# Optimization experiments

Hardware: AMD Instinct MI355X
Metric: run time of the kernel (lower is better)

The kernel has to match this reference:

```python
import jax, jax.numpy as jnp
import numpy as np

B, C, WS, HK = 32, 384, 7, 8           # batch, channels, window size, windows per side
NB, NH, HID = 2, 12, 1536              # num blocks, heads, mlp hidden (4*C)
H = W = HK * WS                        # 56
EPS = 1e-6


def _rel_pos_index(ws: int) -> np.ndarray:
    # Replicates the torch loop: tmp[dy-y+off, dx-x+off] with python negative-index wrap.
    rd = 2 * ws - 1
    a = np.arange(ws)
    qy, qx, ky, kx = np.meshgrid(a, a, a, a, indexing='ij')
    idx = ((ky - qy + ws // 2) % rd) * rd + ((kx - qx + ws // 2) % rd)
    return idx.reshape(ws * ws, ws * ws)


def setup_inputs() -> dict:
    key = jax.random.key(0)
    ks = jax.random.split(key, 12)
    s = 0.02
    inp = {
        'cls_tokens': jax.random.normal(ks[0], (B, C, HK, HK), jnp.float32),
        'patch_tokens': jax.random.normal(ks[1], (B, C, H, W), jnp.float32),
        'qkv_w': s * jax.random.normal(ks[2], (NB, 3 * C, C), jnp.float32),
        'qkv_b': jnp.zeros((NB, 3 * C), jnp.float32),
        'proj_w': s * jax.random.normal(ks[3], (NB, C, C), jnp.float32),
        'proj_b': jnp.zeros((NB, C), jnp.float32),
        'rel_pos': s * jax.random.normal(ks[4], (NB, NH, (2 * WS - 1) ** 2), jnp.float32),
        'ln0_w': jnp.ones((NB, C), jnp.float32), 'ln0_b': jnp.zeros((NB, C), jnp.float32),
        'ln1_w': jnp.ones((NB, C), jnp.float32), 'ln1_b': jnp.zeros((NB, C), jnp.float32),
        'ln2_w': jnp.ones((NB, C), jnp.float32), 'ln2_b': jnp.zeros((NB, C), jnp.float32),
        'mlp_w1': s * jax.random.normal(ks[5], (NB, HID, C), jnp.float32),
        'mlp_b1': jnp.zeros((NB, HID), jnp.float32),
        'mlp_w2': s * jax.random.normal(ks[6], (NB, C, HID), jnp.float32),
        'mlp_b2': jnp.zeros((NB, C), jnp.float32),
    }
    return inp


def _ln(x, w, b):
    m = x.mean(-1, keepdims=True)
    v = ((x - m) ** 2).mean(-1, keepdims=True)
    return (x - m) * jax.lax.rsqrt(v + EPS) * w + b


def _forward(cls_tokens, patch_tokens, qkv_w, qkv_b, proj_w, proj_b, rel_pos,
             ln0_w, ln0_b, ln1_w, ln1_b, ln2_w, ln2_b, mlp_w1, mlp_b1, mlp_w2, mlp_b2):
    hd = C // NH
    scale = hd ** -0.5
    NP = WS * WS  # patch tokens per window

    idx = _rel_pos_index(WS)                                 # [49,49] static
    rp = rel_pos[:, :, idx.reshape(-1)].reshape(NB, NH, NP, NP)
    rp = jnp.pad(rp, ((0, 0), (0, 0), (1, 0), (1, 0)))       # zero bias on cls row/col

    # Projection is Identity (in==out channels, pool=False).
    # convert_to_flatten_layout (no padding needed: H % (HK*WS) == 0)
    p = patch_tokens.reshape(B, C, HK, WS, HK, WS).transpose(0, 2, 4, 3, 5, 1)
    p = p.reshape(B * HK * HK, NP, C)                        # [Bw, 49, C]
    c = cls_tokens.transpose(0, 2, 3, 1).reshape(B * HK * HK, 1, C)
    out = jnp.concatenate([c, p], axis=1)                    # [Bw, 50, C]

    def attn(x, i, patch_attn):
        bx, n, _ = x.shape
        qkv = (x @ qkv_w[i].T + qkv_b[i]).reshape(bx, n, 3, NH, hd).transpose(2, 0, 3, 1, 4)
        q, k, v = qkv[0], qkv[1], qkv[2]
        a = jnp.einsum('bhnd,bhmd->bhnm', q, k) * scale
        if patch_attn:
            a = a + rp[i]
        a = jax.nn.softmax(a, axis=-1)
        o = jnp.einsum('bhnm,bhmd->bhnd', a, v).transpose(0, 2, 1, 3).reshape(bx, n, C)
        return o @ proj_w[i].T + proj_b[i]

    for i in range(NB):
        # cls-token (region) attention across windows of one image
        ct = out[:, 0:1, :].reshape(B, HK * HK, C)
        ct = ct + attn(_ln(ct, ln0_w[i], ln0_b[i]), i, False)
        out = jnp.concatenate([ct.reshape(-1, 1, C), out[:, 1:, :]], axis=1)
        # windowed attention with rel-pos bias
        out = out + attn(_ln(out, ln1_w[i], ln1_b[i]), i, True)
        # MLP (expand is Identity since in==out channels)
        h = _ln(out, ln2_w[i], ln2_b[i])
        h = jax.nn.gelu(h @ mlp_w1[i].T + mlp_b1[i], approximate=False)
        out = out + (h @ mlp_w2[i].T + mlp_b2[i])

    # convert_to_spatial_layout
    cls_out = out[:, 0].reshape(B, HK, HK, C).transpose(0, 3, 1, 2)
    patch_out = out[:, 1:].reshape(B, HK, HK, WS, WS, C).transpose(0, 5, 1, 3, 2, 4).reshape(B, C, H, W)
    return cls_out, patch_out


def reference(cls_tokens, patch_tokens, qkv_w, qkv_b, proj_w, proj_b, rel_pos,
              ln0_w, ln0_b, ln1_w, ln1_b, ln2_w, ln2_b, mlp_w1, mlp_b1, mlp_w2, mlp_b2):
    return _forward(cls_tokens, patch_tokens, qkv_w, qkv_b, proj_w, proj_b, rel_pos,
                    ln0_w, ln0_b, ln1_w, ln1_b, ln2_w, ln2_b, mlp_w1, mlp_b1, mlp_w2, mlp_b2)
```

## Files before the change

kernel.cpp:

```cpp
#include <hip/hip_runtime.h>
#include <hip/hip_bf16.h>
#include <cstdint>
#include <cstddef>

#define BB    32
#define CC    384
#define NHH   12
#define HDD   32
#define WSS   7
#define HKK   8
#define NBB   2
#define HIDD  1536
#define NTT   50
#define NWW   2048
#define LDOUT 19200
#define N3    1152

typedef __attribute__((ext_vector_type(8))) short short8v;
typedef __attribute__((ext_vector_type(4))) float f32x4;

#if defined(__has_builtin)
#if __has_builtin(__builtin_amdgcn_global_load_lds)
#define HAS_GLDS 1
#endif
#endif
#ifndef HAS_GLDS
#define HAS_GLDS 0
#endif

static __device__ __forceinline__ float gelu_f(float x) {
    float t = x * (0.7978845608028654f + 0.03567740814f * x * x);
    float e = __expf(2.0f * t);
    float th = 1.0f - 2.0f / (e + 1.0f);
    return 0.5f * x * (1.0f + th);
}

static __device__ __forceinline__ short bf16s(float x) {
    __hip_bfloat16 b = __float2bfloat16(x);
    return *(short*)&b;
}

static __device__ __forceinline__ float bf2f(short s) {
    union { unsigned int u; float f; } cv;
    cv.u = ((unsigned int)(unsigned short)s) << 16;
    return cv.f;
}

#if HAS_GLDS
static __device__ __forceinline__ void glds16(const short* g, short* l) {
    __builtin_amdgcn_global_load_lds(
        (const __attribute__((address_space(1))) unsigned int*)g,
        (__attribute__((address_space(3))) unsigned int*)l,
        16, 0, 0);
}
#endif

static __device__ __forceinline__ void swz_decode(int L, int nx, int ny, int& bx, int& by) {
    if (ny & 7) {
        bx = L % nx; by = L / nx;
    } else {
        int r = L & 7, pos = L >> 3;
        bx = pos % nx;
        by = (pos / nx) * 8 + r;
    }
}

__global__ void pack_cls_kernel(const float* __restrict__ cls, __hip_bfloat16* __restrict__ out) {
    __shared__ float lds[64][65];
    int bid = blockIdx.x;
    int b = bid / 6, cc = bid % 6, c0 = cc * 64;
    int tid = threadIdx.x;
    for (int idx = tid; idx < 64 * 64; idx += 256) {
        int k = idx & 63, cl = idx >> 6;
        lds[cl][k] = cls[((size_t)b * CC + c0 + cl) * 64 + k];
    }
    __syncthreads();
    short* ob = (short*)out;
    for (int idx = tid; idx < 64 * 64; idx += 256) {
        int cl = idx & 63, k = idx >> 6;
        ob[(size_t)(b * 64 + k) * LDOUT + c0 + cl] = bf16s(lds[cl][k]);
    }
}

__global__ void pack_patch_kernel(const float* __restrict__ patch, __hip_bfloat16* __restrict__ out) {
    __shared__ float lds[64][57];
    int bid = blockIdx.x;
    int b = bid / 336, rem = bid % 336;
    int y = rem / 6, cc = rem % 6, c0 = cc * 64;
    int tid = threadIdx.x;
    for (int idx = tid; idx < 64 * 56; idx += 256) {
        int cl = idx / 56, x = idx % 56;
        lds[cl][x] = patch[(((size_t)b * CC + c0 + cl) * 56 + y) * 56 + x];
    }
    __syncthreads();
    int wsy = y % 7, hky = y / 7;
    short* ob = (short*)out;
    for (int idx = tid; idx < 64 * 56; idx += 256) {
        int cl = idx & 63, x = idx >> 6;
        int tok = 1 + wsy * 7 + (x % 7);
        int win = b * 64 + hky * 8 + (x / 7);
        ob[((size_t)win * NTT + tok) * CC + c0 + cl] = bf16s(lds[cl][x]);
    }
}

__global__ void unpack_cls_kernel(const __hip_bfloat16* __restrict__ out, float* __restrict__ cls_out) {
    __shared__ float lds[64][65];
    int bid = blockIdx.x;
    int b = bid / 6, cc = bid % 6, c0 = cc * 64;
    int tid = threadIdx.x;
    const short* ob = (const short*)out;
    for (int idx = tid; idx < 64 * 64; idx += 256) {
        int cl = idx & 63, k = idx >> 6;
        lds[cl][k] = bf2f(ob[(size_t)(b * 64 + k) * LDOUT + c0 + cl]);
    }
    __syncthreads();
    for (int idx = tid; idx < 64 * 64; idx += 256) {
        int k = idx & 63, cl = idx >> 6;
        cls_out[((size_t)b * CC + c0 + cl) * 64 + k] = lds[cl][k];
    }
}

__global__ void unpack_patch_kernel(const __hip_bfloat16* __restrict__ out, float* __restrict__ patch_out) {
    __shared__ float lds[64][57];
    int bid = blockIdx.x;
    int b = bid / 336, rem = bid % 336;
    int y = rem / 6, cc = rem % 6, c0 = cc * 64;
    int tid = threadIdx.x;
    int wsy = y % 7, hky = y / 7;
    const short* ob = (const short*)out;
    for (int idx = tid; idx < 64 * 56; idx += 256) {
        int cl = idx & 63, x = idx >> 6;
        int tok = 1 + wsy * 7 + (x % 7);
        int win = b * 64 + hky * 8 + (x / 7);
        lds[cl][x] = bf2f(ob[((size_t)win * NTT + tok) * CC + c0 + cl]);
    }
    __syncthreads();
    for (int idx = tid; idx < 64 * 56; idx += 256) {
        int cl = idx / 56, x = idx % 56;
        patch_out[((size_t)b * CC + c0 + cl) * 3136 + y * 56 + x] = lds[cl][x];
    }
}

__global__ void f2bf_kernel(const float* __restrict__ in, __hip_bfloat16* __restrict__ out, int n) {
    int i = (blockIdx.x * 256 + threadIdx.x) * 4;
    if (i + 3 < n) {
        float4 v = *(const float4*)(in + i);
        out[i + 0] = __float2bfloat16(v.x);
        out[i + 1] = __float2bfloat16(v.y);
        out[i + 2] = __float2bfloat16(v.z);
        out[i + 3] = __float2bfloat16(v.w);
    } else {
        for (; i < n; ++i) out[i] = __float2bfloat16(in[i]);
    }
}

__global__ void bias_precompute_kernel(const float* __restrict__ rp, float* __restrict__ biasT) {
    int h = blockIdx.x;
    for (int idx = threadIdx.x; idx < 4096; idx += 256) {
        int qt = idx >> 6, kt = idx & 63;
        float v = 0.f;
        if (qt >= 1 && qt < NTT && kt >= 1 && kt < NTT) {
            int qp = qt - 1, kp = kt - 1;
            int qy = qp / 7, qx = qp - qy * 7;
            int ky = kp / 7, kx = kp - ky * 7;
            int ridx = ((ky - qy + 16) % 13) * 13 + ((kx - qx + 16) % 13);
            v = rp[h * 169 + ridx];
        }
        biasT[h * 4096 + qt * 64 + (kt & 15) * 4 + (kt >> 4)] = v;
    }
}

__global__ void ln_kernel(const __hip_bfloat16* __restrict__ x, int ldx,
                          const float* __restrict__ w, const float* __restrict__ b,
                          __hip_bfloat16* __restrict__ y, int ldy, int M) {
    int wave = threadIdx.x >> 6, lane = threadIdx.x & 63;
    int row = blockIdx.x * 4 + wave;
    if (row >= M) return;
    const ushort2* xr = (const ushort2*)((const short*)x + (size_t)row * ldx);
    float2 vals[3];
    float s = 0.f;
#pragma unroll
    for (int j = 0; j < 3; ++j) {
        ushort2 u = xr[lane + j * 64];
        vals[j].x = bf2f((short)u.x);
        vals[j].y = bf2f((short)u.y);
        s += vals[j].x + vals[j].y;
    }
#pragma unroll
    for (int off = 32; off > 0; off >>= 1) s += __shfl_xor(s, off);
    float mean = s * (1.0f / 384.0f);
    float vs = 0.f;
#pragma unroll
    for (int j = 0; j < 3; ++j) {
        float dx = vals[j].x - mean, dy = vals[j].y - mean;
        vs += dx * dx + dy * dy;
    }
#pragma unroll
    for (int off = 32; off > 0; off >>= 1) vs += __shfl_xor(vs, off);
    float inv = rsqrtf(vs * (1.0f / 384.0f) + 1e-6f);
    const float2* w2 = (const float2*)w;
    const float2* b2 = (const float2*)b;
    ushort* yr = (ushort*)y + (size_t)row * ldy;
#pragma unroll
    for (int j = 0; j < 3; ++j) {
        int c = lane + j * 64;
        float2 wv = w2[c], bv = b2[c];
        ushort2 o;
        o.x = (ushort)bf16s((vals[j].x - mean) * inv * wv.x + bv.x);
        o.y = (ushort)bf16s((vals[j].y - mean) * inv * wv.y + bv.y);
        *(ushort2*)(yr + c * 2) = o;
    }
}

template <int BIAS, int GELU, int ACC>
__global__ __launch_bounds__(512, 4) void gemm_bf16_kernel(
    const __hip_bfloat16* __restrict__ A, int lda,
    const __hip_bfloat16* __restrict__ W,
    const float* __restrict__ bias,
    __hip_bfloat16* __restrict__ Yb, int ldyb,
    int M, int N, int K, int nx) {
    __shared__ __align__(16) union SMemU {
        struct { short As[3][256 * 32]; short Bs[3][128 * 32]; } st;
        short obf[256][132];
    } sm;
    int tid = threadIdx.x;
    int lane = tid & 63;
    int wid = tid >> 6;
    int wr = wid >> 1, wc = wid & 1;
    int bx, by;
    swz_decode(blockIdx.x, nx, M >> 8, bx, by);
    int row0 = by * 256, col0 = bx * 128;

    const short* Ag = (const short*)A + (size_t)(row0 + wid * 32 + (lane >> 2)) * lda + (lane & 3) * 8;
    const short* Wg = (const short*)W + (size_t)(col0 + wid * 16 + (lane >> 2)) * K + (lane & 3) * 8;
    size_t astep16 = (size_t)16 * lda;
    int ldsA = wid * 32 * 32;
    int ldsB = wid * 16 * 32;

#if HAS_GLDS
#define STAGE(buf, k0)                                                \
    do {                                                              \
        glds16(Ag + (k0), &sm.st.As[buf][ldsA]);                      \
        glds16(Ag + astep16 + (k0), &sm.st.As[buf][ldsA + 16 * 32]);  \
        glds16(Wg + (k0), &sm.st.Bs[buf][ldsB]);                      \
    } while (0)
#else
#define STAGE(buf, k0)                                                               \
    do {                                                                             \
        *(short8v*)(&sm.st.As[buf][ldsA] + lane * 8) = *(const short8v*)(Ag + (k0)); \
        *(short8v*)(&sm.st.As[buf][ldsA + 16 * 32] + lane * 8) = *(const short8v*)(Ag + astep16 + (k0)); \
        *(short8v*)(&sm.st.Bs[buf][ldsB] + lane * 8) = *(const short8v*)(Wg + (k0)); \
    } while (0)
#endif

    f32x4 acc[4][4] = {};
    int frow_a = wr * 64 + (lane & 15);
    int frow_b = wc * 64 + (lane & 15);
    int fk = (lane >> 4) * 8;

    int nt = K >> 5;
#if HAS_GLDS
    STAGE(0, 0);
    if (nt > 1) STAGE(1, 32);
    int sc = 0;
    for (int t = 0; t < nt; ++t) {
        int sn = sc + 2; if (sn >= 3) sn -= 3;
        if (t + 2 < nt) {
            STAGE(sn, (t + 2) << 5);
            asm volatile("s_waitcnt vmcnt(6)" ::: "memory");
        } else if (t + 1 < nt) {
            asm volatile("s_waitcnt vmcnt(3)" ::: "memory");
        } else {
            asm volatile("s_waitcnt vmcnt(0)" ::: "memory");
        }
        __builtin_amdgcn_s_barrier();
        __builtin_amdgcn_sched_barrier(0);
        short8v a[4], b[4];
#pragma unroll
        for (int m = 0; m < 4; ++m) a[m] = *(const short8v*)&sm.st.As[sc][(frow_a + m * 16) * 32 + fk];
#pragma unroll
        for (int n = 0; n < 4; ++n) b[n] = *(const short8v*)&sm.st.Bs[sc][(frow_b + n * 16) * 32 + fk];
        __builtin_amdgcn_s_setprio(1);
#pragma unroll
        for (int m = 0; m < 4; ++m)
#pragma unroll
            for (int n = 0; n < 4; ++n)
                acc[m][n] = __builtin_amdgcn_mfma_f32_16x16x32_bf16(a[m], b[n], acc[m][n], 0, 0, 0);
        __builtin_amdgcn_s_setprio(0);
        __builtin_amdgcn_sched_barrier(0);
        __builtin_amdgcn_s_barrier();
        ++sc; if (sc >= 3) sc = 0;
    }
#else
    STAGE(0, 0);
    __syncthreads();
    int cur = 0;
    for (int t = 0; t < nt; ++t) {
        if (t + 1 < nt) STAGE(cur ^ 1, (t + 1) << 5);
        short8v a[4], b[4];
#pragma unroll
        for (int m = 0; m < 4; ++m) a[m] = *(const short8v*)&sm.st.As[cur][(frow_a + m * 16) * 32 + fk];
#pragma unroll
        for (int n = 0; n < 4; ++n) b[n] = *(const short8v*)&sm.st.Bs[cur][(frow_b + n * 16) * 32 + fk];
#pragma unroll
        for (int m = 0; m < 4; ++m)
#pragma unroll
            for (int n = 0; n < 4; ++n)
                acc[m][n] = __builtin_amdgcn_mfma_f32_16x16x32_bf16(a[m], b[n], acc[m][n], 0, 0, 0);
        if (t + 1 < nt) { __syncthreads(); cur ^= 1; }
    }
#endif
#undef STAGE

    __syncthreads();
    int lr = (lane >> 4) * 4;
    int lc = lane & 15;
#pragma unroll
    for (int n = 0; n < 4; ++n) {
        int c = wc * 64 + n * 16 + lc;
        float bv = BIAS ? bias[col0 + c] : 0.0f;
#pragma unroll
        for (int m = 0; m < 4; ++m) {
#pragma unroll
            for (int j = 0; j < 4; ++j) {
                float v = acc[m][n][j] + bv;
                if (GELU) v = gelu_f(v);
                sm.obf[wr * 64 + m * 16 + lr + j][c] = bf16s(v);
            }
        }
    }
    __syncthreads();
    short* yb = (short*)Yb + (size_t)row0 * ldyb + col0;
#pragma unroll
    for (int it = 0; it < 8; ++it) {
        int r = (tid >> 4) + it * 32;
        int c8 = (tid & 15) * 8;
        short8v v = *(const short8v*)&sm.obf[r][c8];
        short* yp = yb + (size_t)r * ldyb + c8;
        if (ACC) {
            short8v o = *(const short8v*)yp;
#pragma unroll
            for (int e = 0; e < 8; ++e) v[e] = bf16s(bf2f(v[e]) + bf2f(o[e]));
        }
        *(short8v*)yp = v;
    }
}

__global__ __launch_bounds__(256) void attn_mfma_kernel(
    const __hip_bfloat16* __restrict__ qkv,
    const float* __restrict__ biasT,
    __hip_bfloat16* __restrict__ o,
    int T, float scale, int nwin) {
    __shared__ __align__(16) short Vt[4][32][72];
    __shared__ __align__(16) short Pl[4][64][40];
    const int tid = threadIdx.x, lane = tid & 63, wv = tid >> 6;
    int p, hg;
    {
        int L = blockIdx.x;
        if (nwin & 7) { hg = L % 3; p = L / 3; }
        else { int r = L & 7, pos = L >> 3; hg = pos % 3; p = (pos / 3) * 8 + r; }
    }
    const int h = hg * 4 + wv;
    const short* q_base = (const short*)qkv + (size_t)p * T * N3;

    const int fr = lane & 15;
    const int fk = (lane >> 4) * 8;
    const int lg = lane >> 4;
    const int lc = lane & 15;

    short8v aq[4], bk[4];
#pragma unroll
    for (int m = 0; m < 4; ++m) {
        const short* qp = q_base + (size_t)(m * 16 + fr) * N3 + h * 32 + fk;
        aq[m] = *(const short8v*)qp;
        bk[m] = *(const short8v*)(qp + 384);
    }

    for (int ch = lane; ch < T * 4; ch += 64) {
        int t = ch >> 2, cq = ch & 3;
        short8v v8 = *(const short8v*)(q_base + (size_t)t * N3 + 768 + h * 32 + cq * 8);
#pragma unroll
        for (int e = 0; e < 8; ++e) Vt[wv][cq * 8 + e][t] = v8[e];
    }
    for (int idx = lane; idx < (64 - T) * 32; idx += 64) {
        int t = T + (idx >> 5), d = idx & 31;
        Vt[wv][d][t] = 0;
    }

    f32x4 acc[4][4] = {};
#pragma unroll
    for (int m = 0; m < 4; ++m)
#pragma unroll
        for (int n = 0; n < 4; ++n)
            acc[m][n] = __builtin_amdgcn_mfma_f32_16x16x32_bf16(aq[m], bk[n], acc[m][n], 0, 0, 0);

    const float* bh = biasT ? (biasT + (size_t)h * 4096) : nullptr;
    float p2[4][4], p3[4][4];
#pragma unroll
    for (int m = 0; m < 4; ++m) {
#pragma unroll
        for (int j = 0; j < 4; ++j) {
            int r = m * 16 + lg * 4 + j;
            float v[4];
            if (bh) {
                float4 bv4 = *(const float4*)(bh + r * 64 + lc * 4);
#pragma unroll
                for (int n = 0; n < 4; ++n) v[n] = acc[m][n][j] * scale + ((const float*)&bv4)[n];
            } else {
#pragma unroll
                for (int n = 0; n < 4; ++n) v[n] = acc[m][n][j] * scale;
            }
#pragma unroll
            for (int n = 0; n < 4; ++n)
                if (n * 16 + lc >= T) v[n] = -1e30f;
            float mx = fmaxf(fmaxf(v[0], v[1]), fmaxf(v[2], v[3]));
#pragma unroll
            for (int off = 1; off < 16; off <<= 1) mx = fmaxf(mx, __shfl_xor(mx, off));
            float s = 0.f;
#pragma unroll
            for (int n = 0; n < 4; ++n) { v[n] = __expf(v[n] - mx); s += v[n]; }
#pragma unroll
            for (int off = 1; off < 16; off <<= 1) s += __shfl_xor(s, off);
            float inv = 1.0f / s;
            Pl[wv][r][lc]      = bf16s(v[0] * inv);
            Pl[wv][r][16 + lc] = bf16s(v[1] * inv);
            p2[m][j] = v[2] * inv;
            p3[m][j] = v[3] * inv;
        }
    }

    f32x4 oacc[4][2] = {};
    {
        short8v ap[4], bv[2];
#pragma unroll
        for (int m = 0; m < 4; ++m) ap[m] = *(const short8v*)&Pl[wv][m * 16 + fr][fk];
#pragma unroll
        for (int n = 0; n < 2; ++n) bv[n] = *(const short8v*)&Vt[wv][n * 16 + fr][fk];
#pragma unroll
        for (int m = 0; m < 4; ++m)
#pragma unroll
            for (int n = 0; n < 2; ++n)
                oacc[m][n] = __builtin_amdgcn_mfma_f32_16x16x32_bf16(ap[m], bv[n], oacc[m][n], 0, 0, 0);
    }
#pragma unroll
    for (int m = 0; m < 4; ++m)
#pragma unroll
        for (int j = 0; j < 4; ++j) {
            int r = m * 16 + lg * 4 + j;
            Pl[wv][r][lc]      = bf16s(p2[m][j]);
            Pl[wv][r][16 + lc] = bf16s(p3[m][j]);
        }
    {
        short8v ap[4], bv[2];
#pragma unroll
        for (int m = 0; m < 4; ++m) ap[m] = *(const short8v*)&Pl[wv][m * 16 + fr][fk];
#pragma unroll
        for (int n = 0; n < 2; ++n) bv[n] = *(const short8v*)&Vt[wv][n * 16 + fr][32 + fk];
#pragma unroll
        for (int m = 0; m < 4; ++m)
#pragma unroll
            for (int n = 0; n < 2; ++n)
                oacc[m][n] = __builtin_amdgcn_mfma_f32_16x16x32_bf16(ap[m], bv[n], oacc[m][n], 0, 0, 0);
    }

    short* ob = (short*)o;
#pragma unroll
    for (int m = 0; m < 4; ++m)
#pragma unroll
        for (int j = 0; j < 4; ++j) {
            int r = m * 16 + lg * 4 + j;
            if (r < T) {
#pragma unroll
                for (int n = 0; n < 2; ++n)
                    ob[((size_t)p * T + r) * CC + h * 32 + n * 16 + lc] = bf16s(oacc[m][n][j]);
            }
        }
}

extern "C" void kernel_launch(void* const* d_in, const int* in_sizes, int n_in,
                              void* d_out, int out_size, void* d_ws, size_t ws_size,
                              hipStream_t stream) {
    const float* cls_in   = (const float*)d_in[0];
    const float* patch_in = (const float*)d_in[1];
    const float* qkv_w    = (const float*)d_in[2];
    const float* qkv_b    = (const float*)d_in[3];
    const float* proj_w   = (const float*)d_in[4];
    const float* proj_b   = (const float*)d_in[5];
    const float* rel_pos  = (const float*)d_in[6];
    const float* ln0w = (const float*)d_in[7];
    const float* ln0b = (const float*)d_in[8];
    const float* ln1w = (const float*)d_in[9];
    const float* ln1b = (const float*)d_in[10];
    const float* ln2w = (const float*)d_in[11];
    const float* ln2b = (const float*)d_in[12];
    const float* w1 = (const float*)d_in[13];
    const float* b1 = (const float*)d_in[14];
    const float* w2 = (const float*)d_in[15];
    const float* b2 = (const float*)d_in[16];

    float* WS = (float*)d_ws;
    size_t avail = ws_size / 4;

    const size_t OUT_FB = 19660800;
    const size_t WB_F   = 1769472;
    const size_t BT_F   = 49152;
    __hip_bfloat16* OUTB = (__hip_bfloat16*)WS;
    __hip_bfloat16* WB = (__hip_bfloat16*)(WS + OUT_FB);
    __hip_bfloat16* qwb = WB;
    __hip_bfloat16* pwb = WB + 884736;
    __hip_bfloat16* w1b = WB + 1179648;
    __hip_bfloat16* w2b = WB + 2359296;
    float* biasTbuf = WS + OUT_FB + WB_F;

    int cw = 1024;
    while (cw > 128 && OUT_FB + WB_F + BT_F + (size_t)cw * 48000 > avail) cw >>= 1;
    float* fbase = WS + OUT_FB + WB_F + BT_F;
    __hip_bfloat16* Xb = (__hip_bfloat16*)fbase;
    __hip_bfloat16* Qb = (__hip_bfloat16*)(fbase + (size_t)cw * 9600);
    __hip_bfloat16* Hb = Qb;
    const float scale = 0.17677669529663687f;

    f2bf_kernel<<<dim3((884736 / 4 + 255) / 256), dim3(256), 0, stream>>>(qkv_w, qwb, 884736);
    f2bf_kernel<<<dim3((294912 / 4 + 255) / 256), dim3(256), 0, stream>>>(proj_w, pwb, 294912);
    f2bf_kernel<<<dim3((1179648 / 4 + 255) / 256), dim3(256), 0, stream>>>(w1, w1b, 1179648);
    f2bf_kernel<<<dim3((1179648 / 4 + 255) / 256), dim3(256), 0, stream>>>(w2, w2b, 1179648);

    pack_cls_kernel<<<dim3(BB * 6), dim3(256), 0, stream>>>(cls_in, OUTB);
    pack_patch_kernel<<<dim3(BB * 56 * 6), dim3(256), 0, stream>>>(patch_in, OUTB);

    for (int i = 0; i < NBB; ++i) {
        const __hip_bfloat16* qw = qwb + (size_t)i * N3 * CC;
        const float* qb = qkv_b + (size_t)i * N3;
        const __hip_bfloat16* pw = pwb + (size_t)i * CC * CC;
        const float* pb = proj_b + (size_t)i * CC;
        const float* rp = rel_pos + (size_t)i * NHH * 169;
        const __hip_bfloat16* w1i = w1b + (size_t)i * HIDD * CC;
        const float* b1i = b1 + (size_t)i * HIDD;
        const __hip_bfloat16* w2i = w2b + (size_t)i * CC * HIDD;
        const float* b2i = b2 + (size_t)i * CC;

        bias_precompute_kernel<<<dim3(NHH), dim3(256), 0, stream>>>(rp, biasTbuf);

        ln_kernel<<<dim3(2048 / 4), dim3(256), 0, stream>>>(OUTB, LDOUT, ln0w + i * CC, ln0b + i * CC, Xb, CC, 2048);
        gemm_bf16_kernel<1, 0, 0><<<dim3((N3 / 128) * (2048 / 256)), dim3(512), 0, stream>>>(
            Xb, CC, qw, qb, Qb, N3, 2048, N3, CC, N3 / 128);
        attn_mfma_kernel<<<dim3(BB * 3), dim3(256), 0, stream>>>(Qb, nullptr, Xb, 64, scale, BB);
        gemm_bf16_kernel<1, 0, 1><<<dim3((CC / 128) * (2048 / 256)), dim3(512), 0, stream>>>(
            Xb, CC, pw, pb, OUTB, LDOUT, 2048, CC, CC, CC / 128);

        for (int w0 = 0; w0 < NWW; w0 += cw) {
            __hip_bfloat16* outc = OUTB + (size_t)w0 * LDOUT;
            int Mr = cw * NTT;
            ln_kernel<<<dim3(Mr / 4), dim3(256), 0, stream>>>(outc, CC, ln1w + i * CC, ln1b + i * CC, Xb, CC, Mr);
            gemm_bf16_kernel<1, 0, 0><<<dim3((N3 / 128) * (Mr / 256)), dim3(512), 0, stream>>>(
                Xb, CC, qw, qb, Qb, N3, Mr, N3, CC, N3 / 128);
            attn_mfma_kernel<<<dim3(cw * 3), dim3(256), 0, stream>>>(Qb, biasTbuf, Xb, NTT, scale, cw);
            gemm_bf16_kernel<1, 0, 1><<<dim3((CC / 128) * (Mr / 256)), dim3(512), 0, stream>>>(
                Xb, CC, pw, pb, outc, CC, Mr, CC, CC, CC / 128);
        }

        for (int w0 = 0; w0 < NWW; w0 += cw) {
            __hip_bfloat16* outc = OUTB + (size_t)w0 * LDOUT;
            int Mr = cw * NTT;
            ln_kernel<<<dim3(Mr / 4), dim3(256), 0, stream>>>(outc, CC, ln2w + i * CC, ln2b + i * CC, Xb, CC, Mr);
            gemm_bf16_kernel<1, 1, 0><<<dim3((HIDD / 128) * (Mr / 256)), dim3(512), 0, stream>>>(
                Xb, CC, w1i, b1i, Hb, HIDD, Mr, HIDD, CC, HIDD / 128);
            gemm_bf16_kernel<1, 0, 1><<<dim3((CC / 128) * (Mr / 256)), dim3(512), 0, stream>>>(
                Hb, HIDD, w2i, b2i, outc, CC, Mr, CC, HIDD, CC / 128);
        }
    }

    unpack_cls_kernel<<<dim3(BB * 6), dim3(256), 0, stream>>>(OUTB, (float*)d_out);
    unpack_patch_kernel<<<dim3(BB * 56 * 6), dim3(256), 0, stream>>>(OUTB, (float*)d_out + 786432);
}
```

Baseline: 1.913 ms.

## Use BK=64 double-buffered LDS tiles with XOR swizzle in bf16 GEMM

```diff
diff --git a/kernel.cpp b/kernel.cpp
--- a/kernel.cpp
+++ b/kernel.cpp
@@ -213,14 +213,14 @@
 }
 
 template <int BIAS, int GELU, int ACC>
-__global__ __launch_bounds__(512, 4) void gemm_bf16_kernel(
+__global__ __launch_bounds__(512, 2) void gemm_bf16_kernel(
     const __hip_bfloat16* __restrict__ A, int lda,
     const __hip_bfloat16* __restrict__ W,
     const float* __restrict__ bias,
     __hip_bfloat16* __restrict__ Yb, int ldyb,
     int M, int N, int K, int nx) {
     __shared__ __align__(16) union SMemU {
-        struct { short As[3][256 * 32]; short Bs[3][128 * 32]; } st;
+        struct { short As[2][256 * 64]; short Bs[2][128 * 64]; } st;
         short obf[256][132];
     } sm;
     int tid = threadIdx.x;
@@ -231,83 +231,97 @@
     swz_decode(blockIdx.x, nx, M >> 8, bx, by);
     int row0 = by * 256, col0 = bx * 128;
 
-    const short* Ag = (const short*)A + (size_t)(row0 + wid * 32 + (lane >> 2)) * lda + (lane & 3) * 8;
-    const short* Wg = (const short*)W + (size_t)(col0 + wid * 16 + (lane >> 2)) * K + (lane & 3) * 8;
-    size_t astep16 = (size_t)16 * lda;
-    int ldsA = wid * 32 * 32;
-    int ldsB = wid * 16 * 32;
+    int srow8 = lane >> 3;
+    int sgrp  = ((lane & 7) ^ srow8) * 8;
+    const short* Ag = (const short*)A + (size_t)(row0 + wid * 32 + srow8) * lda + sgrp;
+    const short* Wg = (const short*)W + (size_t)(col0 + wid * 16 + srow8) * K + sgrp;
+    int ldsA = wid * 32 * 64;
+    int ldsB = wid * 16 * 64;
 
 #if HAS_GLDS
-#define STAGE(buf, k0)                                                \
-    do {                                                              \
-        glds16(Ag + (k0), &sm.st.As[buf][ldsA]);                      \
-        glds16(Ag + astep16 + (k0), &sm.st.As[buf][ldsA + 16 * 32]);  \
-        glds16(Wg + (k0), &sm.st.Bs[buf][ldsB]);                      \
+#define STAGE(buf, k0)                                                        \
+    do {                                                                      \
+        glds16(Ag + (k0),                &sm.st.As[buf][ldsA]);               \
+        glds16(Ag + 8 * lda + (k0),      &sm.st.As[buf][ldsA + 8 * 64]);      \
+        glds16(Ag + 16 * lda + (k0),     &sm.st.As[buf][ldsA + 16 * 64]);     \
+        glds16(Ag + 24 * lda + (k0),     &sm.st.As[buf][ldsA + 24 * 64]);     \
+        glds16(Wg + (k0),                &sm.st.Bs[buf][ldsB]);               \
+        glds16(Wg + 8 * (size_t)K + (k0), &sm.st.Bs[buf][ldsB + 8 * 64]);     \
     } while (0)
 #else
-#define STAGE(buf, k0)                                                               \
-    do {                                                                             \
-        *(short8v*)(&sm.st.As[buf][ldsA] + lane * 8) = *(const short8v*)(Ag + (k0)); \
-        *(short8v*)(&sm.st.As[buf][ldsA + 16 * 32] + lane * 8) = *(const short8v*)(Ag + astep16 + (k0)); \
-        *(short8v*)(&sm.st.Bs[buf][ldsB] + lane * 8) = *(const short8v*)(Wg + (k0)); \
+#define STAGE(buf, k0)                                                                     \
+    do {                                                                                   \
+        *(short8v*)(&sm.st.As[buf][ldsA] + lane * 8) = *(const short8v*)(Ag + (k0));       \
+        *(short8v*)(&sm.st.As[buf][ldsA + 8 * 64] + lane * 8) = *(const short8v*)(Ag + 8 * lda + (k0)); \
+        *(short8v*)(&sm.st.As[buf][ldsA + 16 * 64] + lane * 8) = *(const short8v*)(Ag + 16 * lda + (k0)); \
+        *(short8v*)(&sm.st.As[buf][ldsA + 24 * 64] + lane * 8) = *(const short8v*)(Ag + 24 * lda + (k0)); \
+        *(short8v*)(&sm.st.Bs[buf][ldsB] + lane * 8) = *(const short8v*)(Wg + (k0));       \
+        *(short8v*)(&sm.st.Bs[buf][ldsB + 8 * 64] + lane * 8) = *(const short8v*)(Wg + 8 * (size_t)K + (k0)); \
     } while (0)
 #endif
 
     f32x4 acc[4][4] = {};
-    int frow_a = wr * 64 + (lane & 15);
-    int frow_b = wc * 64 + (lane & 15);
-    int fk = (lane >> 4) * 8;
-
-    int nt = K >> 5;
+    int swzk[2];
+#pragma unroll
+    for (int kh = 0; kh < 2; ++kh)
+        swzk[kh] = ((((lane >> 4) + kh * 4) ^ (lane & 7)) * 8);
+    int arow[4], brow[4];
+#pragma unroll
+    for (int f = 0; f < 4; ++f) {
+        arow[f] = (wr * 64 + f * 16 + (lane & 15)) * 64;
+        brow[f] = (wc * 64 + f * 16 + (lane & 15)) * 64;
+    }
+
+    int nt = K >> 6;
 #if HAS_GLDS
     STAGE(0, 0);
-    if (nt > 1) STAGE(1, 32);
     int sc = 0;
     for (int t = 0; t < nt; ++t) {
-        int sn = sc + 2; if (sn >= 3) sn -= 3;
-        if (t + 2 < nt) {
-            STAGE(sn, (t + 2) << 5);
+        if (t + 1 < nt) {
+            STAGE(sc ^ 1, (t + 1) << 6);
             asm volatile("s_waitcnt vmcnt(6)" ::: "memory");
-        } else if (t + 1 < nt) {
-            asm volatile("s_waitcnt vmcnt(3)" ::: "memory");
         } else {
             asm volatile("s_waitcnt vmcnt(0)" ::: "memory");
         }
         __builtin_amdgcn_s_barrier();
         __builtin_amdgcn_sched_barrier(0);
-        short8v a[4], b[4];
-#pragma unroll
-        for (int m = 0; m < 4; ++m) a[m] = *(const short8v*)&sm.st.As[sc][(frow_a + m * 16) * 32 + fk];
-#pragma unroll
-        for (int n = 0; n < 4; ++n) b[n] = *(const short8v*)&sm.st.Bs[sc][(frow_b + n * 16) * 32 + fk];
-        __builtin_amdgcn_s_setprio(1);
-#pragma unroll
-        for (int m = 0; m < 4; ++m)
-#pragma unroll
-            for (int n = 0; n < 4; ++n)
-                acc[m][n] = __builtin_amdgcn_mfma_f32_16x16x32_bf16(a[m], b[n], acc[m][n], 0, 0, 0);
-        __builtin_amdgcn_s_setprio(0);
+#pragma unroll
+        for (int kh = 0; kh < 2; ++kh) {
+            short8v a[4], b[4];
+#pragma unroll
+            for (int m = 0; m < 4; ++m) a[m] = *(const short8v*)&sm.st.As[sc][arow[m] + swzk[kh]];
+#pragma unroll
+            for (int n = 0; n < 4; ++n) b[n] = *(const short8v*)&sm.st.Bs[sc][brow[n] + swzk[kh]];
+            __builtin_amdgcn_s_setprio(1);
+#pragma unroll
+            for (int m = 0; m < 4; ++m)
+#pragma unroll
+                for (int n = 0; n < 4; ++n)
+                    acc[m][n] = __builtin_amdgcn_mfma_f32_16x16x32_bf16(a[m], b[n], acc[m][n], 0, 0, 0);
+            __builtin_amdgcn_s_setprio(0);
+        }
         __builtin_amdgcn_sched_barrier(0);
         __builtin_amdgcn_s_barrier();
-        ++sc; if (sc >= 3) sc = 0;
+        sc ^= 1;
     }
 #else
-    STAGE(0, 0);
-    __syncthreads();
-    int cur = 0;
     for (int t = 0; t < nt; ++t) {
-        if (t + 1 < nt) STAGE(cur ^ 1, (t + 1) << 5);
-        short8v a[4], b[4];
-#pragma unroll
-        for (int m = 0; m < 4; ++m) a[m] = *(const short8v*)&sm.st.As[cur][(frow_a + m * 16) * 32 + fk];
-#pragma unroll
-        for (int n = 0; n < 4; ++n) b[n] = *(const short8v*)&sm.st.Bs[cur][(frow_b + n * 16) * 32 + fk];
-#pragma unroll
-        for (int m = 0; m < 4; ++m)
-#pragma unroll
-            for (int n = 0; n < 4; ++n)
-                acc[m][n] = __builtin_amdgcn_mfma_f32_16x16x32_bf16(a[m], b[n], acc[m][n], 0, 0, 0);
-        if (t + 1 < nt) { __syncthreads(); cur ^= 1; }
+        STAGE(0, t << 6);
+        __syncthreads();
+#pragma unroll
+        for (int kh = 0; kh < 2; ++kh) {
+            short8v a[4], b[4];
+#pragma unroll
+            for (int m = 0; m < 4; ++m) a[m] = *(const short8v*)&sm.st.As[0][arow[m] + swzk[kh]];
+#pragma unroll
+            for (int n = 0; n < 4; ++n) b[n] = *(const short8v*)&sm.st.Bs[0][brow[n] + swzk[kh]];
+#pragma unroll
+            for (int m = 0; m < 4; ++m)
+#pragma unroll
+                for (int n = 0; n < 4; ++n)
+                    acc[m][n] = __builtin_amdgcn_mfma_f32_16x16x32_bf16(a[m], b[n], acc[m][n], 0, 0, 0);
+        }
+        __syncthreads();
     }
 #endif
 #undef STAGE
```

After: 2.049 ms. +7.1%, slower.
